# Kernel tuning notes

Hardware: AMD Instinct MI355X
Metric: run time of the kernel (lower is better)

## Reference

```python
import jax, jax.numpy as jnp
import numpy as np
import math

B, T, D, H = 4, 2048, 2048, 16
HD = D // H  # 128


def rotate_half(x):
    half = x.shape[-1] // 2
    return jnp.concatenate([-x[..., half:], x[..., :half]], axis=-1)


def apply_rope(x, cos, sin):
    # x: [B,H,T,hd]; cos/sin: [T,hd] -> broadcast over B,H
    return x * cos[None, None] + rotate_half(x) * sin[None, None]


def setup_inputs() -> dict:
    key = jax.random.key(0)
    ks = jax.random.split(key, 6)
    x = jax.random.normal(ks[0], (B, T, D), dtype=jnp.float32)
    # standard RoPE tables
    inv_freq = 1.0 / (10000.0 ** (np.arange(0, HD, 2, dtype=np.float32) / HD))
    freqs = np.arange(T, dtype=np.float32)[:, None] * inv_freq[None, :]  # [T, hd/2]
    emb = np.concatenate([freqs, freqs], axis=-1)  # [T, hd]
    cos = jnp.asarray(np.cos(emb))
    sin = jnp.asarray(np.sin(emb))
    # additive causal mask [T,T]: 0 on/below diagonal, -1e9 above
    mask = jnp.where(jnp.tril(jnp.ones((T, T), dtype=bool)), 0.0, -1e9).astype(jnp.float32)
    scale = 0.02
    Wq = scale * jax.random.normal(ks[1], (D, D), dtype=jnp.float32)
    Wk = scale * jax.random.normal(ks[2], (D, D), dtype=jnp.float32)
    Wv = scale * jax.random.normal(ks[3], (D, D), dtype=jnp.float32)
    Wo = scale * jax.random.normal(ks[4], (D, D), dtype=jnp.float32)
    return {"x": x, "cos": cos, "sin": sin, "mask": mask,
            "Wq": Wq, "Wk": Wk, "Wv": Wv, "Wo": Wo}


def reference(x, cos, sin, mask, Wq, Wk, Wv, Wo):
    b, t, d = x.shape

    def split_heads(y):  # [B,T,D] -> [B,H,T,hd]
        return y.reshape(b, t, H, HD).transpose(0, 2, 1, 3)

    # nn.Linear: y = x @ W.T
    Q = apply_rope(split_heads(jnp.einsum('btd,od->bto', x, Wq)), cos, sin)
    K = apply_rope(split_heads(jnp.einsum('btd,od->bto', x, Wk)), cos, sin)
    V = split_heads(jnp.einsum('btd,od->bto', x, Wv))

    scores = jnp.einsum('bhqd,bhkd->bhqk', Q, K) / math.sqrt(HD)
    scores = scores + mask  # [T,T] broadcasts over [B,H,T,T]
    weights = jax.nn.softmax(scores, axis=-1)
    out = jnp.einsum('bhqk,bhkd->bhqd', weights, V)
    out = out.transpose(0, 2, 1, 3).reshape(b, t, d)
    return jnp.einsum('btd,od->bto', out, Wo)
```

## Files before the change

### kernel.cpp

```cpp
#include <hip/hip_runtime.h>
#include <hip/hip_bf16.h>

#define DEV static __device__ __forceinline__

typedef __attribute__((ext_vector_type(8))) _Float16 half8;
typedef __attribute__((ext_vector_type(4))) float f32x4;

constexpr int Bc = 4, Tc = 2048, Dc = 2048, Hc = 16;

DEV ushort f2h(float f) { _Float16 h = (_Float16)f; return __builtin_bit_cast(ushort, h); }
DEV float  h2f(ushort u) { return (float)__builtin_bit_cast(_Float16, u); }

DEV f32x4 MFMA(half8 a, half8 b, f32x4 c) {
  return __builtin_amdgcn_mfma_f32_16x16x32_f16(a, b, c, 0, 0, 0);
}

DEV void async_cp16(void* lds, const void* g) {
  __builtin_amdgcn_global_load_lds((const __attribute__((address_space(1))) void*)g,
                                   (__attribute__((address_space(3))) void*)lds,
                                   16, 0, 0);
}

__global__ __launch_bounds__(256) void cvt(const float* __restrict__ in,
                                           ushort* __restrict__ out, int n4) {
  const int i = blockIdx.x * 256 + threadIdx.x;
  if (i >= n4) return;
  const float4 v = ((const float4*)in)[i];
  ushort4 o;
  o.x = f2h(v.x); o.y = f2h(v.y); o.z = f2h(v.z); o.w = f2h(v.w);
  ((ushort4*)out)[i] = o;
}

template <typename OutT>
__global__ __launch_bounds__(512, 2) void gemm256(const ushort* __restrict__ A,
                                                  const ushort* __restrict__ Bw,
                                                  OutT* __restrict__ C) {
  __shared__ ushort As[4][256 * 32];
  __shared__ ushort Bs[4][256 * 32];
  const int tid = threadIdx.x;
  const int lane = tid & 63, wid = tid >> 6;
  const int g = lane >> 4, q16 = lane & 15;
  const int wm = wid >> 2, wn = wid & 3;

  const int flat = (int)blockIdx.x;
  const int xcd = flat & 7, idx = flat >> 3;
  const int bm = xcd * 4 + (idx & 3);
  const int bn = idx >> 2;
  const ushort* Ab = A + (size_t)bm * 256 * Dc;
  const ushort* Bb = Bw + (size_t)bn * 256 * Dc;

#define STAGE1(KT, BUF, PH) do {                                               \
    const int pass_ = (PH) & 1;                                                \
    const int c_ = pass_ * 512 + tid;                                          \
    const int row_ = c_ >> 2, gl_ = c_ & 3;                                    \
    const int col_ = (KT) * 32 + ((gl_ ^ ((row_ >> 1) & 3)) << 3);             \
    if ((PH) < 2)                                                              \
      async_cp16(&As[BUF][(pass_ * 512 + wid * 64) * 8],                       \
                 Ab + (size_t)row_ * Dc + col_);                               \
    else                                                                       \
      async_cp16(&Bs[BUF][(pass_ * 512 + wid * 64) * 8],                       \
                 Bb + (size_t)row_ * Dc + col_);                               \
  } while (0)

  f32x4 acc[8][4] = {};

  for (int tt = 0; tt < 3; ++tt) {
    STAGE1(tt, tt, 0); STAGE1(tt, tt, 1);
    STAGE1(tt, tt, 2); STAGE1(tt, tt, 3);
  }
  asm volatile("s_waitcnt vmcnt(0)" ::: "memory");
  __builtin_amdgcn_s_barrier();
  __builtin_amdgcn_sched_barrier(0);

  const int sgz = (g ^ ((q16 >> 1) & 3)) << 3;

#define PHASE(AA, BB, RDA, RDB, PH) do {                                       \
    if (RDA) {                                                                 \
      _Pragma("unroll") for (int mf_ = 0; mf_ < 4; ++mf_) {                    \
        const int r_ = wm * 128 + (AA) * 64 + mf_ * 16 + q16;                  \
        af[mf_] = *(const half8*)&Asb[r_ * 32 + sgz];                          \
      }                                                                        \
    }                                                                          \
    if (RDB) {                                                                 \
      _Pragma("unroll") for (int nf_ = 0; nf_ < 2; ++nf_) {                    \
        const int r_ = wn * 64 + (BB) * 32 + nf_ * 16 + q16;                   \
        bf[nf_] = *(const half8*)&Bsb[r_ * 32 + sgz];                          \
      }                                                                        \
    }                                                                          \
    if (st) STAGE1(t + 3, sb, PH);                                             \
    asm volatile("s_waitcnt vmcnt(8)" ::: "memory");                           \
    __builtin_amdgcn_s_barrier();                                              \
    __builtin_amdgcn_sched_barrier(0);                                         \
    __builtin_amdgcn_s_setprio(1);                                             \
    _Pragma("unroll") for (int mf_ = 0; mf_ < 4; ++mf_)                        \
      _Pragma("unroll") for (int nf_ = 0; nf_ < 2; ++nf_)                      \
        acc[(AA) * 4 + mf_][(BB) * 2 + nf_] =                                  \
            MFMA(af[mf_], bf[nf_], acc[(AA) * 4 + mf_][(BB) * 2 + nf_]);       \
    __builtin_amdgcn_s_setprio(0);                                             \
  } while (0)

#pragma unroll 1
  for (int t = 0; t < 64; ++t) {
    const int rb = t & 3;
    const int sb = (t + 3) & 3;
    const bool st = (t + 3) < 64;
    const ushort* Asb = As[rb];
    const ushort* Bsb = Bs[rb];
    half8 af[4], bf[2];
    PHASE(0, 0, 1, 1, 0);
    PHASE(0, 1, 0, 1, 1);
    PHASE(1, 1, 1, 0, 2);
    PHASE(1, 0, 0, 1, 3);
  }
#undef PHASE
#undef STAGE1

  const int m00 = bm * 256 + wm * 128 + g * 4;
  const int n0 = bn * 256 + wn * 64 + q16;
#pragma unroll
  for (int mf = 0; mf < 8; ++mf)
#pragma unroll
    for (int nf = 0; nf < 4; ++nf) {
      const int m0 = m00 + mf * 16;
      const int n = n0 + nf * 16;
#pragma unroll
      for (int r = 0; r < 4; ++r) {
        const float v = acc[mf][nf][r];
        if constexpr (sizeof(OutT) == 2)
          C[(size_t)(m0 + r) * Dc + n] = (OutT)f2h(v);
        else
          C[(size_t)(m0 + r) * Dc + n] = (OutT)v;
      }
    }
}

__global__ __launch_bounds__(256) void rope(ushort* __restrict__ X,
                                            const float* __restrict__ cs,
                                            const float* __restrict__ sn) {
  const int tid = blockIdx.x * 256 + threadIdx.x;
  const int row = tid >> 4;
  const int jq = (tid & 15) << 2;
  const int t = (row >> 4) & (Tc - 1);
  ushort* base = X + (size_t)row * 128;
  const ushort4 lo = *(const ushort4*)(base + jq);
  const ushort4 hi = *(const ushort4*)(base + 64 + jq);
  const float4 c4 = *(const float4*)(cs + t * 128 + jq);
  const float4 s4 = *(const float4*)(sn + t * 128 + jq);
  const float xl[4] = {h2f(lo.x), h2f(lo.y), h2f(lo.z), h2f(lo.w)};
  const float xh[4] = {h2f(hi.x), h2f(hi.y), h2f(hi.z), h2f(hi.w)};
  const float cc[4] = {c4.x, c4.y, c4.z, c4.w};
  const float ss[4] = {s4.x, s4.y, s4.z, s4.w};
  ushort4 olo, ohi;
  ushort* po = (ushort*)&olo;
  ushort* ph = (ushort*)&ohi;
#pragma unroll
  for (int k = 0; k < 4; ++k) {
    po[k] = f2h(xl[k] * cc[k] - xh[k] * ss[k]);
    ph[k] = f2h(xh[k] * cc[k] + xl[k] * ss[k]);
  }
  *(ushort4*)(base + jq) = olo;
  *(ushort4*)(base + 64 + jq) = ohi;
}

__global__ __launch_bounds__(512, 2) void attn(const ushort* __restrict__ Q,
                                               const ushort* __restrict__ K,
                                               const ushort* __restrict__ V,
                                               ushort* __restrict__ O) {
  __shared__ ushort Ks[2][64 * 128];
  __shared__ ushort Vt[2][128 * 64];

  const int tid = threadIdx.x;
  const int lane = tid & 63, wid = tid >> 6;
  const int g = lane >> 4, q16 = lane & 15;

  const int flat = (int)(blockIdx.x + 4 * blockIdx.y);
  const int xcd = flat & 7, idx = flat >> 3;
  const int bh = xcd + 8 * (idx & 7);
  const int pr = idx >> 3;

  const int b = bh >> 4, h = bh & 15;
  const size_t headbase = ((size_t)b * Tc * Hc + h) * 128;
  const float SCL2 = 0.12751743f;

  const int vdc = (wid & 3) * 4 + (lane & 3);
  const int vkvp = (wid >> 2) * 16 + (lane >> 2);

  uint4 vreg[2];

#define ISSUEK(KT, BUF) do {                                                   \
    const ushort* Kb_ = K + headbase + (size_t)(KT) * 64 * Dc;                 \
    _Pragma("unroll") for (int i_ = 0; i_ < 2; ++i_) {                         \
      const int c_ = i_ * 512 + tid;                                           \
      const int kv_ = c_ >> 4, gl_ = c_ & 15;                                  \
      async_cp16(&Ks[BUF][(i_ * 512 + wid * 64) * 8],                          \
                 Kb_ + (size_t)kv_ * Dc + ((gl_ ^ (kv_ & 7)) << 3));           \
    }                                                                          \
  } while (0)

#define LOADV(KT) do {                                                         \
    const ushort* p0_ = V + headbase + (size_t)((KT) * 64 + 2 * vkvp) * Dc +   \
                        vdc * 8;                                               \
    vreg[0] = *(const uint4*)p0_;                                              \
    vreg[1] = *(const uint4*)(p0_ + Dc);                                       \
  } while (0)

#define WRITEV(BUF) do {                                                       \
    const ushort* e0_ = (const ushort*)&vreg[0];                               \
    const ushort* e1_ = (const ushort*)&vreg[1];                               \
    _Pragma("unroll") for (int j_ = 0; j_ < 8; ++j_) {                         \
      const int d_ = vdc * 8 + j_;                                             \
      const unsigned w_ = (unsigned)e0_[j_] | ((unsigned)e1_[j_] << 16);       \
      *(unsigned*)&Vt[BUF][(d_ * 64 + 2 * vkvp) ^ ((d_ & 7) << 3)] = w_;       \
    }                                                                          \
  } while (0)

#pragma unroll 1
  for (int half = 0; half < 2; ++half) {
    const int q0 = (half ? pr : 7 - pr) * 256;
    const int qrow = q0 + wid * 32;
    const int nt = q0 / 64 + 4;

    half8 qreg[2][4];
#pragma unroll
    for (int qf = 0; qf < 2; ++qf)
#pragma unroll
      for (int ds = 0; ds < 4; ++ds)
        qreg[qf][ds] = *(const half8*)(Q + headbase +
                       (size_t)(qrow + qf * 16 + q16) * Dc + ds * 32 + g * 8);

    f32x4 oacc[2][8] = {};
    float m_[2] = {-1e30f, -1e30f};
    float l_[2] = {0.f, 0.f};

    __builtin_amdgcn_s_barrier();
    __builtin_amdgcn_sched_barrier(0);
    ISSUEK(0, 0);
    LOADV(0);
    WRITEV(0);

#pragma unroll 1
    for (int kt = 0; kt < nt; ++kt) {
      const int cur = kt & 1;
      const int kv0 = kt * 64;
      asm volatile("s_waitcnt vmcnt(0) lgkmcnt(0)" ::: "memory");
      __builtin_amdgcn_s_barrier();
      __builtin_amdgcn_sched_barrier(0);
      if (kt + 1 < nt) {
        ISSUEK(kt + 1, cur ^ 1);
        LOADV(kt + 1);
      }

      if (kv0 <= qrow + 31) {
        const ushort* Ksb = Ks[cur];
        const ushort* Vtb = Vt[cur];
        f32x4 s[2][4] = {};
        __builtin_amdgcn_s_setprio(1);
#pragma unroll
        for (int ds = 0; ds < 4; ++ds) {
          half8 kf[4];
#pragma unroll
          for (int kvf = 0; kvf < 4; ++kvf) {
            const int kv = kvf * 16 + q16;
            kf[kvf] = *(const half8*)&Ksb[(kv * 128 + ds * 32 + g * 8) ^ ((kv & 7) << 3)];
          }
#pragma unroll
          for (int kvf = 0; kvf < 4; ++kvf)
#pragma unroll
            for (int qf = 0; qf < 2; ++qf)
              s[qf][kvf] = MFMA(kf[kvf], qreg[qf][ds], s[qf][kvf]);
        }
        __builtin_amdgcn_s_setprio(0);
        float pmax[2] = {-1e30f, -1e30f};
        if (kv0 + 63 > qrow) {
#pragma unroll
          for (int qf = 0; qf < 2; ++qf) {
            const int qg = qrow + qf * 16 + q16;
#pragma unroll
            for (int kvf = 0; kvf < 4; ++kvf)
#pragma unroll
              for (int r = 0; r < 4; ++r) {
                float v = s[qf][kvf][r];
                if ((kv0 + kvf * 16 + g * 4 + r) > qg) v = -1e30f;
                s[qf][kvf][r] = v;
                pmax[qf] = fmaxf(pmax[qf], v);
              }
          }
        } else {
#pragma unroll
          for (int qf = 0; qf < 2; ++qf)
#pragma unroll
            for (int kvf = 0; kvf < 4; ++kvf)
#pragma unroll
              for (int r = 0; r < 4; ++r)
                pmax[qf] = fmaxf(pmax[qf], s[qf][kvf][r]);
        }
#pragma unroll
        for (int qf = 0; qf < 2; ++qf) {
          pmax[qf] = fmaxf(pmax[qf], __shfl_xor(pmax[qf], 16));
          pmax[qf] = fmaxf(pmax[qf], __shfl_xor(pmax[qf], 32));
        }
        if (!__all((pmax[0] <= m_[0] + 16.f) & (pmax[1] <= m_[1] + 16.f))) {
#pragma unroll
          for (int qf = 0; qf < 2; ++qf) {
            const float mn2 = fmaxf(m_[qf], pmax[qf]);
            const float alpha = __builtin_exp2f((m_[qf] - mn2) * SCL2);
            m_[qf] = mn2;
            l_[qf] *= alpha;
#pragma unroll
            for (int df = 0; df < 8; ++df)
              oacc[qf][df] *= alpha;
          }
        }
        uint w[2][4][2];
#pragma unroll
        for (int qf = 0; qf < 2; ++qf) {
          const float mn = m_[qf];
          float lsum = 0.f;
#pragma unroll
          for (int kvf = 0; kvf < 4; ++kvf) {
            const float p0 = __builtin_exp2f((s[qf][kvf][0] - mn) * SCL2);
            const float p1 = __builtin_exp2f((s[qf][kvf][1] - mn) * SCL2);
            const float p2 = __builtin_exp2f((s[qf][kvf][2] - mn) * SCL2);
            const float p3 = __builtin_exp2f((s[qf][kvf][3] - mn) * SCL2);
            lsum += (p0 + p1) + (p2 + p3);
            w[qf][kvf][0] = (unsigned)f2h(p0) | ((unsigned)f2h(p1) << 16);
            w[qf][kvf][1] = (unsigned)f2h(p2) | ((unsigned)f2h(p3) << 16);
          }
          l_[qf] += lsum;
        }
        const bool ghi = g >= 2;
        const bool godd = (g & 1) != 0;
        half8 pb[2][2];
#pragma unroll
        for (int qf = 0; qf < 2; ++qf) {
          uint sA[2][2], sB[2][2];
#pragma unroll
          for (int c = 0; c < 2; ++c)
#pragma unroll
            for (int i = 0; i < 2; ++i) {
              sA[c][i] = ghi ? w[qf][2 * c + 1][i] : w[qf][2 * c][i];
              sB[c][i] = ghi ? w[qf][2 * c][i] : w[qf][2 * c + 1][i];
            }
          uint x16[2][2], x32[2][2], x48[2][2];
#pragma unroll
          for (int c = 0; c < 2; ++c)
#pragma unroll
            for (int i = 0; i < 2; ++i) {
              x16[c][i] = __shfl_xor(sA[c][i], 16);
              x32[c][i] = __shfl_xor(sB[c][i], 32);
              x48[c][i] = __shfl_xor(sB[c][i], 48);
            }
#pragma unroll
          for (int c = 0; c < 2; ++c) {
            uint4 t;
            t.x = godd ? (ghi ? x16[c][0] : x48[c][0]) : (ghi ? x32[c][0] : sA[c][0]);
            t.y = godd ? (ghi ? x16[c][1] : x48[c][1]) : (ghi ? x32[c][1] : sA[c][1]);
            t.z = godd ? (ghi ? sA[c][0] : x32[c][0]) : (ghi ? x48[c][0] : x16[c][0]);
            t.w = godd ? (ghi ? sA[c][1] : x32[c][1]) : (ghi ? x48[c][1] : x16[c][1]);
            pb[qf][c] = __builtin_bit_cast(half8, t);
          }
        }
        __builtin_amdgcn_s_setprio(1);
#pragma unroll
        for (int c = 0; c < 2; ++c) {
#pragma unroll
          for (int df = 0; df < 8; ++df) {
            const int d = df * 16 + q16;
            const half8 vf = *(const half8*)&Vtb[(d * 64 + c * 32 + g * 8) ^ ((d & 7) << 3)];
#pragma unroll
            for (int qf = 0; qf < 2; ++qf)
              oacc[qf][df] = MFMA(vf, pb[qf][c], oacc[qf][df]);
          }
        }
        __builtin_amdgcn_s_setprio(0);
      }

      if (kt + 1 < nt) WRITEV(cur ^ 1);
    }

#pragma unroll
    for (int qf = 0; qf < 2; ++qf) {
      float l = l_[qf];
      l += __shfl_xor(l, 16);
      l += __shfl_xor(l, 32);
      const float inv = 1.0f / l;
      const int t = qrow + qf * 16 + q16;
#pragma unroll
      for (int df = 0; df < 8; ++df) {
        const f32x4 v = oacc[qf][df];
        ushort4 o;
        o.x = f2h(v[0] * inv); o.y = f2h(v[1] * inv);
        o.z = f2h(v[2] * inv); o.w = f2h(v[3] * inv);
        *(ushort4*)(O + headbase + (size_t)t * Dc + df * 16 + g * 4) = o;
      }
    }
  }
#undef ISSUEK
#undef LOADV
#undef WRITEV
}

extern "C" void kernel_launch(void* const* d_in, const int* in_sizes, int n_in,
                              void* d_out, int out_size, void* d_ws, size_t ws_size,
                              hipStream_t stream) {
  (void)in_sizes; (void)n_in; (void)out_size; (void)ws_size;
  const float* x  = (const float*)d_in[0];
  const float* cs = (const float*)d_in[1];
  const float* sn = (const float*)d_in[2];
  const float* Wq = (const float*)d_in[4];
  const float* Wk = (const float*)d_in[5];
  const float* Wv = (const float*)d_in[6];
  const float* Wo = (const float*)d_in[7];
  float* out = (float*)d_out;

  char* ws = (char*)d_ws;
  const size_t MB = 1024 * 1024;
  ushort* xb  = (ushort*)(ws);
  ushort* wqb = (ushort*)(ws + 32 * MB);
  ushort* wkb = (ushort*)(ws + 40 * MB);
  ushort* wvb = (ushort*)(ws + 48 * MB);
  ushort* wob = (ushort*)(ws + 56 * MB);
  ushort* Qr  = (ushort*)(ws + 64 * MB);
  ushort* Kr  = (ushort*)(ws + 96 * MB);
  ushort* Vr  = (ushort*)(ws + 128 * MB);

  cvt<<<16384, 256, 0, stream>>>(x, xb, 4194304);
  cvt<<<4096, 256, 0, stream>>>(Wq, wqb, 1048576);
  cvt<<<4096, 256, 0, stream>>>(Wk, wkb, 1048576);
  cvt<<<4096, 256, 0, stream>>>(Wv, wvb, 1048576);
  cvt<<<4096, 256, 0, stream>>>(Wo, wob, 1048576);

  gemm256<ushort><<<256, 512, 0, stream>>>(xb, wqb, Qr);
  gemm256<ushort><<<256, 512, 0, stream>>>(xb, wkb, Kr);
  gemm256<ushort><<<256, 512, 0, stream>>>(xb, wvb, Vr);

  rope<<<8192, 256, 0, stream>>>(Qr, cs, sn);
  rope<<<8192, 256, 0, stream>>>(Kr, cs, sn);

  attn<<<dim3(4, 64), 512, 0, stream>>>(Qr, Kr, Vr, xb);

  gemm256<float><<<256, 512, 0, stream>>>(xb, wob, out);
}
```

Measured before the change: 509.9 us.

## Split attention into 1024 smaller blocks with 32-wide KV tiles

Restructures the attention kernel from 256 blocks of 512 threads, each handling two paired 256-row query tiles, to 1024 blocks of 256 threads, each handling one 128-row query tile. The query tiles are assigned in a snake order so causal work is balanced across blocks. KV tiles shrink from 64 to 32 rows, which halves LDS per block and allows more resident blocks per CU, and the probability shuffle is simplified to fit. It also switches to packed RTZ half conversion for the probabilities. The risk is more barriers and loop iterations per unit of work, and lower MFMA density per tile.

```diff
diff --git a/kernel.cpp b/kernel.cpp
--- a/kernel.cpp
+++ b/kernel.cpp
@@ -4,12 +4,16 @@
 #define DEV static __device__ __forceinline__
 
 typedef __attribute__((ext_vector_type(8))) _Float16 half8;
+typedef __attribute__((ext_vector_type(2))) _Float16 half2v;
 typedef __attribute__((ext_vector_type(4))) float f32x4;
 
 constexpr int Bc = 4, Tc = 2048, Dc = 2048, Hc = 16;
 
 DEV ushort f2h(float f) { _Float16 h = (_Float16)f; return __builtin_bit_cast(ushort, h); }
 DEV float  h2f(ushort u) { return (float)__builtin_bit_cast(_Float16, u); }
+DEV uint pk2h(float a, float b) {
+  return __builtin_bit_cast(uint, __builtin_amdgcn_cvt_pkrtz(a, b));
+}
 
 DEV f32x4 MFMA(half8 a, half8 b, f32x4 c) {
   return __builtin_amdgcn_mfma_f32_16x16x32_f16(a, b, c, 0, 0, 0);
@@ -162,43 +166,50 @@
   *(ushort4*)(base + 64 + jq) = ohi;
 }
 
-__global__ __launch_bounds__(512, 2) void attn(const ushort* __restrict__ Q,
+__global__ __launch_bounds__(256, 4) void attn(const ushort* __restrict__ Q,
                                                const ushort* __restrict__ K,
                                                const ushort* __restrict__ V,
                                                ushort* __restrict__ O) {
-  __shared__ ushort Ks[2][64 * 128];
-  __shared__ ushort Vt[2][128 * 64];
+  __shared__ ushort Ks[2][32 * 128];
+  __shared__ ushort Vt[2][128 * 32];
 
   const int tid = threadIdx.x;
   const int lane = tid & 63, wid = tid >> 6;
   const int g = lane >> 4, q16 = lane & 15;
 
-  const int flat = (int)(blockIdx.x + 4 * blockIdx.y);
+  const int flat = (int)blockIdx.x;
   const int xcd = flat & 7, idx = flat >> 3;
   const int bh = xcd + 8 * (idx & 7);
-  const int pr = idx >> 3;
+  const int rank = idx >> 3;
+  const int rk = rank >> 2, rb2 = rank & 3;
+  const int qt = (rk == 0) ? (15 - rb2)
+               : (rk == 1) ? rb2
+               : (rk == 2) ? (8 + rb2) : (7 - rb2);
 
   const int b = bh >> 4, h = bh & 15;
   const size_t headbase = ((size_t)b * Tc * Hc + h) * 128;
   const float SCL2 = 0.12751743f;
 
-  const int vdc = (wid & 3) * 4 + (lane & 3);
-  const int vkvp = (wid >> 2) * 16 + (lane >> 2);
+  const int qrow = qt * 128 + wid * 32;
+  const int nt = qt * 4 + 4;
+
+  const int vdc = wid * 4 + (lane & 3);
+  const int vkvp = lane >> 2;
 
   uint4 vreg[2];
 
 #define ISSUEK(KT, BUF) do {                                                   \
-    const ushort* Kb_ = K + headbase + (size_t)(KT) * 64 * Dc;                 \
+    const ushort* Kb_ = K + headbase + (size_t)(KT) * 32 * Dc;                 \
     _Pragma("unroll") for (int i_ = 0; i_ < 2; ++i_) {                         \
-      const int c_ = i_ * 512 + tid;                                           \
+      const int c_ = i_ * 256 + tid;                                           \
       const int kv_ = c_ >> 4, gl_ = c_ & 15;                                  \
-      async_cp16(&Ks[BUF][(i_ * 512 + wid * 64) * 8],                          \
+      async_cp16(&Ks[BUF][(i_ * 256 + wid * 64) * 8],                          \
                  Kb_ + (size_t)kv_ * Dc + ((gl_ ^ (kv_ & 7)) << 3));           \
     }                                                                          \
   } while (0)
 
 #define LOADV(KT) do {                                                         \
-    const ushort* p0_ = V + headbase + (size_t)((KT) * 64 + 2 * vkvp) * Dc +   \
+    const ushort* p0_ = V + headbase + (size_t)((KT) * 32 + 2 * vkvp) * Dc +   \
                         vdc * 8;                                               \
     vreg[0] = *(const uint4*)p0_;                                              \
     vreg[1] = *(const uint4*)(p0_ + Dc);                                       \
@@ -210,189 +221,169 @@
     _Pragma("unroll") for (int j_ = 0; j_ < 8; ++j_) {                         \
       const int d_ = vdc * 8 + j_;                                             \
       const unsigned w_ = (unsigned)e0_[j_] | ((unsigned)e1_[j_] << 16);       \
-      *(unsigned*)&Vt[BUF][(d_ * 64 + 2 * vkvp) ^ ((d_ & 7) << 3)] = w_;       \
+      *(unsigned*)&Vt[BUF][(d_ * 32 + 2 * vkvp) ^ ((d_ & 3) << 3)] = w_;       \
     }                                                                          \
   } while (0)
 
+  half8 qreg[2][4];
+#pragma unroll
+  for (int qf = 0; qf < 2; ++qf)
+#pragma unroll
+    for (int ds = 0; ds < 4; ++ds)
+      qreg[qf][ds] = *(const half8*)(Q + headbase +
+                     (size_t)(qrow + qf * 16 + q16) * Dc + ds * 32 + g * 8);
+
+  f32x4 oacc[2][8] = {};
+  float m_[2] = {-1e30f, -1e30f};
+  float l_[2] = {0.f, 0.f};
+
+  ISSUEK(0, 0);
+  LOADV(0);
+  WRITEV(0);
+
 #pragma unroll 1
-  for (int half = 0; half < 2; ++half) {
-    const int q0 = (half ? pr : 7 - pr) * 256;
-    const int qrow = q0 + wid * 32;
-    const int nt = q0 / 64 + 4;
-
-    half8 qreg[2][4];
-#pragma unroll
-    for (int qf = 0; qf < 2; ++qf)
-#pragma unroll
-      for (int ds = 0; ds < 4; ++ds)
-        qreg[qf][ds] = *(const half8*)(Q + headbase +
-                       (size_t)(qrow + qf * 16 + q16) * Dc + ds * 32 + g * 8);
-
-    f32x4 oacc[2][8] = {};
-    float m_[2] = {-1e30f, -1e30f};
-    float l_[2] = {0.f, 0.f};
-
+  for (int kt = 0; kt < nt; ++kt) {
+    const int cur = kt & 1;
+    const int kv0 = kt * 32;
+    asm volatile("s_waitcnt vmcnt(0) lgkmcnt(0)" ::: "memory");
     __builtin_amdgcn_s_barrier();
     __builtin_amdgcn_sched_barrier(0);
-    ISSUEK(0, 0);
-    LOADV(0);
-    WRITEV(0);
-
-#pragma unroll 1
-    for (int kt = 0; kt < nt; ++kt) {
-      const int cur = kt & 1;
-      const int kv0 = kt * 64;
-      asm volatile("s_waitcnt vmcnt(0) lgkmcnt(0)" ::: "memory");
-      __builtin_amdgcn_s_barrier();
-      __builtin_amdgcn_sched_barrier(0);
-      if (kt + 1 < nt) {
-        ISSUEK(kt + 1, cur ^ 1);
-        LOADV(kt + 1);
-      }
-
-      if (kv0 <= qrow + 31) {
-        const ushort* Ksb = Ks[cur];
-        const ushort* Vtb = Vt[cur];
-        f32x4 s[2][4] = {};
-        __builtin_amdgcn_s_setprio(1);
-#pragma unroll
-        for (int ds = 0; ds < 4; ++ds) {
-          half8 kf[4];
-#pragma unroll
-          for (int kvf = 0; kvf < 4; ++kvf) {
-            const int kv = kvf * 16 + q16;
-            kf[kvf] = *(const half8*)&Ksb[(kv * 128 + ds * 32 + g * 8) ^ ((kv & 7) << 3)];
-          }
-#pragma unroll
-          for (int kvf = 0; kvf < 4; ++kvf)
-#pragma unroll
-            for (int qf = 0; qf < 2; ++qf)
-              s[qf][kvf] = MFMA(kf[kvf], qreg[qf][ds], s[qf][kvf]);
+    if (kt + 1 < nt) {
+      ISSUEK(kt + 1, cur ^ 1);
+      LOADV(kt + 1);
+    }
+
+    if (kv0 <= qrow + 31) {
+      const ushort* Ksb = Ks[cur];
+      const ushort* Vtb = Vt[cur];
+      f32x4 s[2][2] = {};
+      __builtin_amdgcn_s_setprio(1);
+#pragma unroll
+      for (int ds = 0; ds < 4; ++ds) {
+        half8 kf[2];
+#pragma unroll
+        for (int kvf = 0; kvf < 2; ++kvf) {
+          const int kv = kvf * 16 + q16;
+          kf[kvf] = *(const half8*)&Ksb[(kv * 128 + ds * 32 + g * 8) ^ ((kv & 7) << 3)];
         }
-        __builtin_amdgcn_s_setprio(0);
-        float pmax[2] = {-1e30f, -1e30f};
-        if (kv0 + 63 > qrow) {
-#pragma unroll
-          for (int qf = 0; qf < 2; ++qf) {
-            const int qg = qrow + qf * 16 + q16;
-#pragma unroll
-            for (int kvf = 0; kvf < 4; ++kvf)
-#pragma unroll
-              for (int r = 0; r < 4; ++r) {
-                float v = s[qf][kvf][r];
-                if ((kv0 + kvf * 16 + g * 4 + r) > qg) v = -1e30f;
-                s[qf][kvf][r] = v;
-                pmax[qf] = fmaxf(pmax[qf], v);
-              }
-          }
-        } else {
+#pragma unroll
+        for (int kvf = 0; kvf < 2; ++kvf)
 #pragma unroll
           for (int qf = 0; qf < 2; ++qf)
-#pragma unroll
-            for (int kvf = 0; kvf < 4; ++kvf)
-#pragma unroll
-              for (int r = 0; r < 4; ++r)
-                pmax[qf] = fmaxf(pmax[qf], s[qf][kvf][r]);
+            s[qf][kvf] = MFMA(kf[kvf], qreg[qf][ds], s[qf][kvf]);
+      }
+      __builtin_amdgcn_s_setprio(0);
+      float pmax[2] = {-1e30f, -1e30f};
+      if (kv0 + 31 > qrow) {
+#pragma unroll
+        for (int qf = 0; qf < 2; ++qf) {
+          const int qg = qrow + qf * 16 + q16;
+#pragma unroll
+          for (int kvf = 0; kvf < 2; ++kvf)
+#pragma unroll
+            for (int r = 0; r < 4; ++r) {
+              float v = s[qf][kvf][r];
+              if ((kv0 + kvf * 16 + g * 4 + r) > qg) v = -1e30f;
+              s[qf][kvf][r] = v;
+              pmax[qf] = fmaxf(pmax[qf], v);
+            }
         }
+      } else {
+#pragma unroll
+        for (int qf = 0; qf < 2; ++qf)
+#pragma unroll
+          for (int kvf = 0; kvf < 2; ++kvf)
+#pragma unroll
+            for (int r = 0; r < 4; ++r)
+              pmax[qf] = fmaxf(pmax[qf], s[qf][kvf][r]);
+      }
+#pragma unroll
+      for (int qf = 0; qf < 2; ++qf) {
+        pmax[qf] = fmaxf(pmax[qf], __shfl_xor(pmax[qf], 16));
+        pmax[qf] = fmaxf(pmax[qf], __shfl_xor(pmax[qf], 32));
+      }
+      if (!__all((pmax[0] <= m_[0] + 16.f) & (pmax[1] <= m_[1] + 16.f))) {
 #pragma unroll
         for (int qf = 0; qf < 2; ++qf) {
-          pmax[qf] = fmaxf(pmax[qf], __shfl_xor(pmax[qf], 16));
-          pmax[qf] = fmaxf(pmax[qf], __shfl_xor(pmax[qf], 32));
+          const float mn2 = fmaxf(m_[qf], pmax[qf]);
+          const float alpha = __builtin_exp2f((m_[qf] - mn2) * SCL2);
+          m_[qf] = mn2;
+          l_[qf] *= alpha;
+#pragma unroll
+          for (int df = 0; df < 8; ++df)
+            oacc[qf][df] *= alpha;
         }
-        if (!__all((pmax[0] <= m_[0] + 16.f) & (pmax[1] <= m_[1] + 16.f))) {
-#pragma unroll
-          for (int qf = 0; qf < 2; ++qf) {
-            const float mn2 = fmaxf(m_[qf], pmax[qf]);
-            const float alpha = __builtin_exp2f((m_[qf] - mn2) * SCL2);
-            m_[qf] = mn2;
-            l_[qf] *= alpha;
-#pragma unroll
-            for (int df = 0; df < 8; ++df)
-              oacc[qf][df] *= alpha;
-          }
+      }
+      uint w[2][2][2];
+#pragma unroll
+      for (int qf = 0; qf < 2; ++qf) {
+        const float mn = m_[qf];
+        float lsum = 0.f;
+#pragma unroll
+        for (int kvf = 0; kvf < 2; ++kvf) {
+          const float p0 = __builtin_exp2f((s[qf][kvf][0] - mn) * SCL2);
+          const float p1 = __builtin_exp2f((s[qf][kvf][1] - mn) * SCL2);
+          const float p2 = __builtin_exp2f((s[qf][kvf][2] - mn) * SCL2);
+          const float p3 = __builtin_exp2f((s[qf][kvf][3] - mn) * SCL2);
+          lsum += (p0 + p1) + (p2 + p3);
+          w[qf][kvf][0] = pk2h(p0, p1);
+          w[qf][kvf][1] = pk2h(p2, p3);
         }
-        uint w[2][4][2];
-#pragma unroll
-        for (int qf = 0; qf < 2; ++qf) {
-          const float mn = m_[qf];
-          float lsum = 0.f;
-#pragma unroll
-          for (int kvf = 0; kvf < 4; ++kvf) {
-            const float p0 = __builtin_exp2f((s[qf][kvf][0] - mn) * SCL2);
-            const float p1 = __builtin_exp2f((s[qf][kvf][1] - mn) * SCL2);
-            const float p2 = __builtin_exp2f((s[qf][kvf][2] - mn) * SCL2);
-            const float p3 = __builtin_exp2f((s[qf][kvf][3] - mn) * SCL2);
-            lsum += (p0 + p1) + (p2 + p3);
-            w[qf][kvf][0] = (unsigned)f2h(p0) | ((unsigned)f2h(p1) << 16);
-            w[qf][kvf][1] = (unsigned)f2h(p2) | ((unsigned)f2h(p3) << 16);
-          }
-          l_[qf] += lsum;
+        l_[qf] += lsum;
+      }
+      const bool ghi = g >= 2;
+      const bool godd = (g & 1) != 0;
+      half8 pb[2];
+#pragma unroll
+      for (int qf = 0; qf < 2; ++qf) {
+        const uint* w0 = w[qf][0];
+        const uint* w1 = w[qf][1];
+        uint R16[2], R32[2], R48[2];
+#pragma unroll
+        for (int i = 0; i < 2; ++i) {
+          const uint S16 = (g == 1) ? w0[i] : w1[i];
+          const uint S32 = (g == 3) ? w0[i] : w1[i];
+          const uint S48 = (g == 2) ? w0[i] : w1[i];
+          R16[i] = __shfl_xor(S16, 16);
+          R32[i] = __shfl_xor(S32, 32);
+          R48[i] = __shfl_xor(S48, 48);
         }
-        const bool ghi = g >= 2;
-        const bool godd = (g & 1) != 0;
-        half8 pb[2][2];
-#pragma unroll
-        for (int qf = 0; qf < 2; ++qf) {
-          uint sA[2][2], sB[2][2];
-#pragma unroll
-          for (int c = 0; c < 2; ++c)
-#pragma unroll
-            for (int i = 0; i < 2; ++i) {
-              sA[c][i] = ghi ? w[qf][2 * c + 1][i] : w[qf][2 * c][i];
-              sB[c][i] = ghi ? w[qf][2 * c][i] : w[qf][2 * c + 1][i];
-            }
-          uint x16[2][2], x32[2][2], x48[2][2];
-#pragma unroll
-          for (int c = 0; c < 2; ++c)
-#pragma unroll
-            for (int i = 0; i < 2; ++i) {
-              x16[c][i] = __shfl_xor(sA[c][i], 16);
-              x32[c][i] = __shfl_xor(sB[c][i], 32);
-              x48[c][i] = __shfl_xor(sB[c][i], 48);
-            }
-#pragma unroll
-          for (int c = 0; c < 2; ++c) {
-            uint4 t;
-            t.x = godd ? (ghi ? x16[c][0] : x48[c][0]) : (ghi ? x32[c][0] : sA[c][0]);
-            t.y = godd ? (ghi ? x16[c][1] : x48[c][1]) : (ghi ? x32[c][1] : sA[c][1]);
-            t.z = godd ? (ghi ? sA[c][0] : x32[c][0]) : (ghi ? x48[c][0] : x16[c][0]);
-            t.w = godd ? (ghi ? sA[c][1] : x32[c][1]) : (ghi ? x48[c][1] : x16[c][1]);
-            pb[qf][c] = __builtin_bit_cast(half8, t);
-          }
-        }
-        __builtin_amdgcn_s_setprio(1);
-#pragma unroll
-        for (int c = 0; c < 2; ++c) {
-#pragma unroll
-          for (int df = 0; df < 8; ++df) {
-            const int d = df * 16 + q16;
-            const half8 vf = *(const half8*)&Vtb[(d * 64 + c * 32 + g * 8) ^ ((d & 7) << 3)];
-#pragma unroll
-            for (int qf = 0; qf < 2; ++qf)
-              oacc[qf][df] = MFMA(vf, pb[qf][c], oacc[qf][df]);
-          }
-        }
-        __builtin_amdgcn_s_setprio(0);
-      }
-
-      if (kt + 1 < nt) WRITEV(cur ^ 1);
+        uint4 t;
+        t.x = !ghi ? (godd ? R48[0] : w0[0]) : (godd ? R16[0] : R32[0]);
+        t.y = !ghi ? (godd ? R48[1] : w0[1]) : (godd ? R16[1] : R32[1]);
+        t.z = !ghi ? (godd ? R32[0] : R16[0]) : (godd ? w1[0] : R48[0]);
+        t.w = !ghi ? (godd ? R32[1] : R16[1]) : (godd ? w1[1] : R48[1]);
+        pb[qf] = __builtin_bit_cast(half8, t);
+      }
+      __builtin_amdgcn_s_setprio(1);
+#pragma unroll
+      for (int df = 0; df < 8; ++df) {
+        const int d = df * 16 + q16;
+        const half8 vf = *(const half8*)&Vtb[(d * 32 + g * 8) ^ ((d & 3) << 3)];
+#pragma unroll
+        for (int qf = 0; qf < 2; ++qf)
+          oacc[qf][df] = MFMA(vf, pb[qf], oacc[qf][df]);
+      }
+      __builtin_amdgcn_s_setprio(0);
     }
 
-#pragma unroll
-    for (int qf = 0; qf < 2; ++qf) {
-      float l = l_[qf];
-      l += __shfl_xor(l, 16);
-      l += __shfl_xor(l, 32);
-      const float inv = 1.0f / l;
-      const int t = qrow + qf * 16 + q16;
-#pragma unroll
-      for (int df = 0; df < 8; ++df) {
-        const f32x4 v = oacc[qf][df];
-        ushort4 o;
-        o.x = f2h(v[0] * inv); o.y = f2h(v[1] * inv);
-        o.z = f2h(v[2] * inv); o.w = f2h(v[3] * inv);
-        *(ushort4*)(O + headbase + (size_t)t * Dc + df * 16 + g * 4) = o;
-      }
+    if (kt + 1 < nt) WRITEV(cur ^ 1);
+  }
+
+#pragma unroll
+  for (int qf = 0; qf < 2; ++qf) {
+    float l = l_[qf];
+    l += __shfl_xor(l, 16);
+    l += __shfl_xor(l, 32);
+    const float inv = 1.0f / l;
+    const int t = qrow + qf * 16 + q16;
+#pragma unroll
+    for (int df = 0; df < 8; ++df) {
+      const f32x4 v = oacc[qf][df];
+      ushort4 o;
+      o.x = f2h(v[0] * inv); o.y = f2h(v[1] * inv);
+      o.z = f2h(v[2] * inv); o.w = f2h(v[3] * inv);
+      *(ushort4*)(O + headbase + (size_t)t * Dc + df * 16 + g * 4) = o;
     }
   }
 #undef ISSUEK
@@ -437,7 +428,7 @@
   rope<<<8192, 256, 0, stream>>>(Qr, cs, sn);
   rope<<<8192, 256, 0, stream>>>(Kr, cs, sn);
 
-  attn<<<dim3(4, 64), 512, 0, stream>>>(Qr, Kr, Vr, xb);
+  attn<<<1024, 256, 0, stream>>>(Qr, Kr, Vr, xb);
 
   gemm256<float><<<256, 512, 0, stream>>>(xb, wob, out);
 }
```

New measurement: 821.0 us. 1.61x slower.

## Restructure GEMM k-loop into two half-phases with fewer barriers and waits

Applied to the files above, without the earlier changes.

Replaces the four-phase per-k-step schedule (four barriers, four vmcnt waits, eight MFMAs each) with two phases of sixteen MFMAs. All four B fragments are loaded once and reused across both A halves. The prologue now waits only for the first stage, and the loop waits once per k-step with tail-aware vmcnt counts. The aim is to cut synchronisation overhead and redundant LDS reads, at the cost of more live fragment registers and some risk in the new wait and barrier ordering.

```diff
diff --git a/kernel.cpp b/kernel.cpp
--- a/kernel.cpp
+++ b/kernel.cpp
@@ -68,36 +68,11 @@
     STAGE1(tt, tt, 0); STAGE1(tt, tt, 1);
     STAGE1(tt, tt, 2); STAGE1(tt, tt, 3);
   }
-  asm volatile("s_waitcnt vmcnt(0)" ::: "memory");
+  asm volatile("s_waitcnt vmcnt(8)" ::: "memory");
   __builtin_amdgcn_s_barrier();
   __builtin_amdgcn_sched_barrier(0);
 
   const int sgz = (g ^ ((q16 >> 1) & 3)) << 3;
-
-#define PHASE(AA, BB, RDA, RDB, PH) do {                                       \
-    if (RDA) {                                                                 \
-      _Pragma("unroll") for (int mf_ = 0; mf_ < 4; ++mf_) {                    \
-        const int r_ = wm * 128 + (AA) * 64 + mf_ * 16 + q16;                  \
-        af[mf_] = *(const half8*)&Asb[r_ * 32 + sgz];                          \
-      }                                                                        \
-    }                                                                          \
-    if (RDB) {                                                                 \
-      _Pragma("unroll") for (int nf_ = 0; nf_ < 2; ++nf_) {                    \
-        const int r_ = wn * 64 + (BB) * 32 + nf_ * 16 + q16;                   \
-        bf[nf_] = *(const half8*)&Bsb[r_ * 32 + sgz];                          \
-      }                                                                        \
-    }                                                                          \
-    if (st) STAGE1(t + 3, sb, PH);                                             \
-    asm volatile("s_waitcnt vmcnt(8)" ::: "memory");                           \
-    __builtin_amdgcn_s_barrier();                                              \
-    __builtin_amdgcn_sched_barrier(0);                                         \
-    __builtin_amdgcn_s_setprio(1);                                             \
-    _Pragma("unroll") for (int mf_ = 0; mf_ < 4; ++mf_)                        \
-      _Pragma("unroll") for (int nf_ = 0; nf_ < 2; ++nf_)                      \
-        acc[(AA) * 4 + mf_][(BB) * 2 + nf_] =                                  \
-            MFMA(af[mf_], bf[nf_], acc[(AA) * 4 + mf_][(BB) * 2 + nf_]);       \
-    __builtin_amdgcn_s_setprio(0);                                             \
-  } while (0)
 
 #pragma unroll 1
   for (int t = 0; t < 64; ++t) {
@@ -106,13 +81,48 @@
     const bool st = (t + 3) < 64;
     const ushort* Asb = As[rb];
     const ushort* Bsb = Bs[rb];
-    half8 af[4], bf[2];
-    PHASE(0, 0, 1, 1, 0);
-    PHASE(0, 1, 0, 1, 1);
-    PHASE(1, 1, 1, 0, 2);
-    PHASE(1, 0, 0, 1, 3);
+    half8 af0[4], af1[4], bf[4];
+
+#pragma unroll
+    for (int nf = 0; nf < 4; ++nf) {
+      const int r = wn * 64 + nf * 16 + q16;
+      bf[nf] = *(const half8*)&Bsb[r * 32 + sgz];
+    }
+#pragma unroll
+    for (int mf = 0; mf < 4; ++mf) {
+      const int r = wm * 128 + mf * 16 + q16;
+      af0[mf] = *(const half8*)&Asb[r * 32 + sgz];
+    }
+    if (st) { STAGE1(t + 3, sb, 0); STAGE1(t + 3, sb, 1); }
+    __builtin_amdgcn_s_barrier();
+    __builtin_amdgcn_sched_barrier(0);
+    __builtin_amdgcn_s_setprio(1);
+#pragma unroll
+    for (int mf = 0; mf < 4; ++mf)
+#pragma unroll
+      for (int nf = 0; nf < 4; ++nf)
+        acc[mf][nf] = MFMA(af0[mf], bf[nf], acc[mf][nf]);
+    __builtin_amdgcn_s_setprio(0);
+
+#pragma unroll
+    for (int mf = 0; mf < 4; ++mf) {
+      const int r = wm * 128 + 64 + mf * 16 + q16;
+      af1[mf] = *(const half8*)&Asb[r * 32 + sgz];
+    }
+    if (st) { STAGE1(t + 3, sb, 2); STAGE1(t + 3, sb, 3); }
+    if (st)                asm volatile("s_waitcnt vmcnt(8)" ::: "memory");
+    else if (t + 2 < 64)   asm volatile("s_waitcnt vmcnt(4)" ::: "memory");
+    else if (t + 1 < 64)   asm volatile("s_waitcnt vmcnt(0)" ::: "memory");
+    __builtin_amdgcn_s_barrier();
+    __builtin_amdgcn_sched_barrier(0);
+    __builtin_amdgcn_s_setprio(1);
+#pragma unroll
+    for (int mf = 0; mf < 4; ++mf)
+#pragma unroll
+      for (int nf = 0; nf < 4; ++nf)
+        acc[4 + mf][nf] = MFMA(af1[mf], bf[nf], acc[4 + mf][nf]);
+    __builtin_amdgcn_s_setprio(0);
   }
-#undef PHASE
 #undef STAGE1
 
   const int m00 = bm * 256 + wm * 128 + g * 4;
```

Result: faster. 478.2 us (-6.2%).
